# Optimization experiments

Measured on AMD Instinct MI355X. Metric: run time of the kernel, lower is better.

## Reference

```python
import jax, jax.numpy as jnp
import numpy as np
import math

NUM_HEADS = 16
SIZE = 1024
HEAD_SIZE = SIZE // NUM_HEADS
B, S = 2, 2048


def setup_inputs() -> dict:
    key = jax.random.key(0)
    ks = jax.random.split(key, 11)
    sc = 1.0 / math.sqrt(SIZE)
    inp = {
        "q": jax.random.normal(ks[0], (B, S, SIZE), dtype=jnp.float32),
        "k": jax.random.normal(ks[1], (B, S, SIZE), dtype=jnp.float32),
        "v": jax.random.normal(ks[2], (B, S, SIZE), dtype=jnp.float32),
        "Wq": jax.random.normal(ks[3], (SIZE, SIZE), dtype=jnp.float32) * sc,
        "bq": jax.random.normal(ks[4], (SIZE,), dtype=jnp.float32) * sc,
        "Wk": jax.random.normal(ks[5], (SIZE, SIZE), dtype=jnp.float32) * sc,
        "bk": jax.random.normal(ks[6], (SIZE,), dtype=jnp.float32) * sc,
        "Wv": jax.random.normal(ks[7], (SIZE, SIZE), dtype=jnp.float32) * sc,
        "bv": jax.random.normal(ks[8], (SIZE,), dtype=jnp.float32) * sc,
        "Wo": jax.random.normal(ks[9], (SIZE, SIZE), dtype=jnp.float32) * sc,
        "bo": jax.random.normal(ks[10], (SIZE,), dtype=jnp.float32) * sc,
    }
    return inp


def _split_heads(x):
    # [B, S, SIZE] -> [B, H, S, D]
    b, s, _ = x.shape
    return x.reshape(b, s, NUM_HEADS, HEAD_SIZE).transpose(0, 2, 1, 3)


def reference(q, k, v, Wq, bq, Wk, bk, Wv, bv, Wo, bo):
    qh = _split_heads(q @ Wq.T + bq) / math.sqrt(HEAD_SIZE)  # [B,H,S,D]
    kh = _split_heads(k @ Wk.T + bk)
    vh = _split_heads(v @ Wv.T + bv)
    scores = jnp.einsum("bhqd,bhkd->bhqk", qh, kh)  # [B,H,S,S]
    attn = jax.nn.softmax(scores, axis=-1)
    ctx = jnp.einsum("bhqk,bhkd->bhqd", attn, vh)  # [B,H,S,D]
    ctx = ctx.transpose(0, 2, 1, 3).reshape(q.shape[0], -1, SIZE)
    return ctx @ Wo.T + bo
```

## Files before the change

### kernel.cpp

```cpp
#include <hip/hip_runtime.h>
#include <hip/hip_bf16.h>

#define SIZE 1024
#define NH 16
#define HD 64
#define BB 2
#define SS 2048
#define MROWS (BB * SS)
#define QT 128
#define NQT (SS / QT)
#define NKT ((SS / 2) / 64)

using bf16 = __hip_bfloat16;
using frag16 = __attribute__((ext_vector_type(8))) short;
using f32x4 = __attribute__((ext_vector_type(4))) float;
typedef unsigned int u32;

__device__ __forceinline__ void glds16(const bf16* g, bf16* l) {
    __builtin_amdgcn_global_load_lds(
        (const __attribute__((address_space(1))) u32*)g,
        (__attribute__((address_space(3))) u32*)l, 16, 0, 0);
}

__device__ __forceinline__ void cvt_store8(bf16* dst, const float* src) {
    float4 a = *(const float4*)src;
    float4 b = *(const float4*)(src + 4);
    bf16 t[8];
    t[0] = __float2bfloat16(a.x); t[1] = __float2bfloat16(a.y);
    t[2] = __float2bfloat16(a.z); t[3] = __float2bfloat16(a.w);
    t[4] = __float2bfloat16(b.x); t[5] = __float2bfloat16(b.y);
    t[6] = __float2bfloat16(b.z); t[7] = __float2bfloat16(b.w);
    *(uint4*)dst = *(const uint4*)t;
}

__global__ __launch_bounds__(256) void cast_kernel(
    const float* __restrict__ Wq, const float* __restrict__ Wk,
    const float* __restrict__ Wv, const float* __restrict__ Wo,
    const float* __restrict__ q, const float* __restrict__ k,
    const float* __restrict__ v,
    bf16* __restrict__ Wb, bf16* __restrict__ qb,
    bf16* __restrict__ kb, bf16* __restrict__ vb)
{
    const int z = blockIdx.z;
    const float* s; bf16* d; int n;
    switch (z) {
        case 0: s = Wq; d = Wb;                   n = SIZE * SIZE;  break;
        case 1: s = Wk; d = Wb + SIZE * SIZE;     n = SIZE * SIZE;  break;
        case 2: s = Wv; d = Wb + 2 * SIZE * SIZE; n = SIZE * SIZE;  break;
        case 3: s = Wo; d = Wb + 3 * SIZE * SIZE; n = SIZE * SIZE;  break;
        case 4: s = q;  d = qb;                   n = MROWS * SIZE; break;
        case 5: s = k;  d = kb;                   n = MROWS * SIZE; break;
        default: s = v; d = vb;                   n = MROWS * SIZE; break;
    }
    const int i = (blockIdx.x * 256 + threadIdx.x) * 8;
    if (i < n) cvt_store8(d + i, s + i);
}

__device__ __forceinline__ void gemm_body(
    const bf16* __restrict__ X, const bf16* __restrict__ W,
    const float* __restrict__ bias, bf16* __restrict__ Y, float scale, bool vt_mode)
{
    __shared__ __align__(16) bf16 smem[8704];
    bf16* As = smem;
    bf16* Bs = smem + 4096;

    const int tid = threadIdx.x;
    const int wave = tid >> 6;
    const int lane = tid & 63;
    const int lane15 = lane & 15;
    const int quad = lane >> 4;
    const int bm = blockIdx.y * 128;
    const int bn = blockIdx.x * 128;
    const int wm = (wave & 1) * 64;
    const int wn = (wave >> 1) * 64;

    f32x4 acc[4][4];
#pragma unroll
    for (int i = 0; i < 4; i++)
#pragma unroll
        for (int j = 0; j < 4; j++)
            acc[i][j] = (f32x4){0.f, 0.f, 0.f, 0.f};

    const int srow = lane >> 2;
    const int scol = (lane & 3) * 8;

    for (int kt = 0; kt < SIZE / 32; kt++) {
        const int k0 = kt * 32;
        __syncthreads();
#pragma unroll
        for (int n = 0; n < 2; n++) {
            const int c = wave * 2 + n;
            glds16(X + (size_t)(bm + c * 16 + srow) * SIZE + k0 + scol, As + c * 512);
            glds16(W + (size_t)(bn + c * 16 + srow) * SIZE + k0 + scol, Bs + c * 512);
        }
        __syncthreads();

        frag16 a[4], b[4];
#pragma unroll
        for (int mi = 0; mi < 4; mi++)
            a[mi] = *(const frag16*)(As + (wm + mi * 16 + lane15) * 32 + quad * 8);
#pragma unroll
        for (int ni = 0; ni < 4; ni++)
            b[ni] = *(const frag16*)(Bs + (wn + ni * 16 + lane15) * 32 + quad * 8);
#pragma unroll
        for (int mi = 0; mi < 4; mi++)
#pragma unroll
            for (int ni = 0; ni < 4; ni++)
                acc[mi][ni] = __builtin_amdgcn_mfma_f32_16x16x32_bf16(
                    a[mi], b[ni], acc[mi][ni], 0, 0, 0);
    }

    if (!vt_mode) {
#pragma unroll
        for (int ni = 0; ni < 4; ni++) {
            const int col = bn + wn + ni * 16 + lane15;
            const float bv = bias[col];
#pragma unroll
            for (int mi = 0; mi < 4; mi++) {
                const int row = bm + wm + mi * 16 + quad * 4;
#pragma unroll
                for (int r = 0; r < 4; r++)
                    Y[(size_t)(row + r) * SIZE + col] =
                        __float2bfloat16((acc[mi][ni][r] + bv) * scale);
            }
        }
    } else {
        bf16* tr = smem;
        const int bloc = bm >> 11;
        const int s0g = bm & (SS - 1);
#pragma unroll
        for (int p = 0; p < 2; p++) {
            __syncthreads();
            if ((wave >> 1) == p) {
#pragma unroll
                for (int ni = 0; ni < 4; ni++) {
                    const int colp = ni * 16 + lane15;
                    const float bv = bias[bn + p * 64 + colp];
#pragma unroll
                    for (int mi = 0; mi < 4; mi++) {
                        const int row = wm + mi * 16 + quad * 4;
#pragma unroll
                        for (int r = 0; r < 4; r++)
                            tr[colp * 136 + row + r] =
                                __float2bfloat16(acc[mi][ni][r] + bv);
                    }
                }
            }
            __syncthreads();
            const int colp = tid >> 2;
            const int gcol = bn + p * 64 + colp;
            const int hh = gcol >> 6, dd = gcol & (HD - 1);
            bf16* dst = (bf16*)Y + ((size_t)(bloc * NH + hh) * HD + dd) * SS
                        + s0g + (tid & 3) * 32;
            const bf16* src = tr + colp * 136 + (tid & 3) * 32;
#pragma unroll
            for (int j = 0; j < 4; j++)
                *(uint4*)(dst + j * 8) = *(const uint4*)(src + j * 8);
        }
    }
}

__global__ __launch_bounds__(256) void qkv_proj_kernel(
    const bf16* __restrict__ qb, const bf16* __restrict__ kb, const bf16* __restrict__ vb,
    const bf16* __restrict__ Wb,
    const float* __restrict__ bq, const float* __restrict__ bk, const float* __restrict__ bv,
    bf16* __restrict__ qh, bf16* __restrict__ kh, bf16* __restrict__ vt)
{
    const bf16 *X, *W; const float* bi; bf16* Y; float sc; bool vm;
    if (blockIdx.z == 0)      { X = qb; W = Wb;                   bi = bq; Y = qh; sc = 0.125f; vm = false; }
    else if (blockIdx.z == 1) { X = kb; W = Wb + SIZE * SIZE;     bi = bk; Y = kh; sc = 1.0f;   vm = false; }
    else                      { X = vb; W = Wb + 2 * SIZE * SIZE; bi = bv; Y = vt; sc = 1.0f;   vm = true;  }
    gemm_body(X, W, bi, Y, sc, vm);
}

__global__ __launch_bounds__(256) void attn_kernel(
    const bf16* __restrict__ qh, const bf16* __restrict__ kh,
    const bf16* __restrict__ vt, bf16* __restrict__ po, float* __restrict__ pl)
{
    __shared__ __align__(16) bf16 Ks[64][72];
    __shared__ __align__(16) bf16 Vs[64][72];
    __shared__ __align__(16) bf16 Ps[4][32][72];

    const int tid = threadIdx.x;
    const int wave = tid >> 6;
    const int lane = tid & 63;
    const int lane15 = lane & 15;
    const int quad = lane >> 4;

    const int b = blockIdx.z, h = blockIdx.y;
    const int qt = blockIdx.x >> 1;
    const int sh = blockIdx.x & 1;
    const int q0 = qt * QT;

    const size_t baseq = (size_t)b * SS * SIZE + (size_t)h * HD;
    const size_t basev = (size_t)(b * NH + h) * HD * SS;
    const float LOG2E = 1.44269504088896340736f;
    const float OFF = 12.0f * LOG2E;

    frag16 aq[2][2];
#pragma unroll
    for (int m = 0; m < 2; m++) {
        const int qrow = q0 + wave * 32 + m * 16 + lane15;
        const bf16* qp = qh + baseq + (size_t)qrow * SIZE + quad * 8;
        aq[m][0] = *(const frag16*)(qp);
        aq[m][1] = *(const frag16*)(qp + 32);
    }

    frag16 bones;
#pragma unroll
    for (int e = 0; e < 8; e++) bones[e] = (short)0x3F80;

    f32x4 ofrag[2][4], l_frag[2];
#pragma unroll
    for (int m = 0; m < 2; m++) {
        l_frag[m] = (f32x4){0.f, 0.f, 0.f, 0.f};
#pragma unroll
        for (int dt = 0; dt < 4; dt++) ofrag[m][dt] = (f32x4){0.f, 0.f, 0.f, 0.f};
    }

    const int sr = tid >> 3;
    const int sc = (tid & 7) * 8;

    for (int kt = 0; kt < NKT; kt++) {
        const int s0 = sh * (SS / 2) + kt * 64;
        __syncthreads();
        *(uint4*)&Ks[sr][sc]      = *(const uint4*)(kh + baseq + (size_t)(s0 + sr) * SIZE + sc);
        *(uint4*)&Ks[sr + 32][sc] = *(const uint4*)(kh + baseq + (size_t)(s0 + sr + 32) * SIZE + sc);
        *(uint4*)&Vs[sr][sc]      = *(const uint4*)(vt + basev + (size_t)sr * SS + s0 + sc);
        *(uint4*)&Vs[sr + 32][sc] = *(const uint4*)(vt + basev + (size_t)(sr + 32) * SS + s0 + sc);
        __syncthreads();

        frag16 kf[4][2];
#pragma unroll
        for (int nt = 0; nt < 4; nt++) {
            kf[nt][0] = *(const frag16*)&Ks[nt * 16 + lane15][quad * 8];
            kf[nt][1] = *(const frag16*)&Ks[nt * 16 + lane15][32 + quad * 8];
        }
#pragma unroll
        for (int m = 0; m < 2; m++) {
#pragma unroll
            for (int nt = 0; nt < 4; nt++) {
                f32x4 c = (f32x4){0.f, 0.f, 0.f, 0.f};
                c = __builtin_amdgcn_mfma_f32_16x16x32_bf16(kf[nt][0], aq[m][0], c, 0, 0, 0);
                c = __builtin_amdgcn_mfma_f32_16x16x32_bf16(kf[nt][1], aq[m][1], c, 0, 0, 0);
                bf16 p4[4];
#pragma unroll
                for (int r = 0; r < 4; r++)
                    p4[r] = __float2bfloat16(exp2f(fminf(c[r], 30.f) * LOG2E - OFF));
                *(uint2*)&Ps[wave][m * 16 + lane15][nt * 16 + quad * 4] = *(const uint2*)p4;
            }
        }
        __builtin_amdgcn_wave_barrier();

        frag16 ap[2][2];
#pragma unroll
        for (int m = 0; m < 2; m++)
#pragma unroll
            for (int c2 = 0; c2 < 2; c2++)
                ap[m][c2] = *(const frag16*)&Ps[wave][m * 16 + lane15][c2 * 32 + quad * 8];

#pragma unroll
        for (int m = 0; m < 2; m++)
#pragma unroll
            for (int c2 = 0; c2 < 2; c2++)
                l_frag[m] = __builtin_amdgcn_mfma_f32_16x16x32_bf16(
                    ap[m][c2], bones, l_frag[m], 0, 0, 0);

#pragma unroll
        for (int dt = 0; dt < 4; dt++) {
            frag16 bv0 = *(const frag16*)&Vs[dt * 16 + lane15][quad * 8];
            frag16 bv1 = *(const frag16*)&Vs[dt * 16 + lane15][32 + quad * 8];
#pragma unroll
            for (int m = 0; m < 2; m++) {
                ofrag[m][dt] = __builtin_amdgcn_mfma_f32_16x16x32_bf16(ap[m][0], bv0, ofrag[m][dt], 0, 0, 0);
                ofrag[m][dt] = __builtin_amdgcn_mfma_f32_16x16x32_bf16(ap[m][1], bv1, ofrag[m][dt], 0, 0, 0);
            }
        }
    }

    const int pb = ((b * NH + h) * NQT + qt) * 2 + sh;
    if (lane15 == 0) {
        float* plp = pl + (size_t)pb * QT;
#pragma unroll
        for (int m = 0; m < 2; m++)
#pragma unroll
            for (int r = 0; r < 4; r++)
                plp[wave * 32 + m * 16 + quad * 4 + r] = l_frag[m][r];
    }
    bf16* pop = po + (size_t)pb * QT * HD;
#pragma unroll
    for (int m = 0; m < 2; m++)
#pragma unroll
        for (int dt = 0; dt < 4; dt++)
#pragma unroll
            for (int r = 0; r < 4; r++)
                pop[(size_t)(wave * 32 + m * 16 + quad * 4 + r) * HD + dt * 16 + lane15] =
                    __float2bfloat16(ofrag[m][dt][r]);
}

__global__ __launch_bounds__(256) void combine_kernel(
    const bf16* __restrict__ po, const float* __restrict__ pl, bf16* __restrict__ ctx)
{
    const int b = blockIdx.z, h = blockIdx.y, qt = blockIdx.x;
    const int tile = (b * NH + h) * NQT + qt;
    const bf16* p0 = po + (size_t)(tile * 2 + 0) * QT * HD;
    const bf16* p1 = po + (size_t)(tile * 2 + 1) * QT * HD;
    const int qr = threadIdx.x >> 1;
    const int dh = (threadIdx.x & 1) * 32;
    const float l = pl[(size_t)(tile * 2) * QT + qr] + pl[(size_t)(tile * 2 + 1) * QT + qr];
    const float inv = 1.0f / fmaxf(l, 1e-30f);
    bf16* dst = ctx + ((size_t)b * SS + qt * QT + qr) * SIZE + h * HD + dh;
    const bf16* s0p = p0 + qr * HD + dh;
    const bf16* s1p = p1 + qr * HD + dh;
#pragma unroll
    for (int j = 0; j < 32; j += 8) {
        uint4 u0 = *(const uint4*)(s0p + j);
        uint4 u1 = *(const uint4*)(s1p + j);
        const bf16* a = (const bf16*)&u0;
        const bf16* bt = (const bf16*)&u1;
        bf16 o[8];
#pragma unroll
        for (int e = 0; e < 8; e++)
            o[e] = __float2bfloat16((__bfloat162float(a[e]) + __bfloat162float(bt[e])) * inv);
        *(uint4*)(dst + j) = *(const uint4*)o;
    }
}

__global__ __launch_bounds__(256) void out_proj_kernel(
    const bf16* __restrict__ ctx, const bf16* __restrict__ Wob,
    const float* __restrict__ bo, float* __restrict__ out)
{
    __shared__ __align__(16) bf16 As[64 * 32];
    __shared__ __align__(16) bf16 Bs[128 * 32];

    const int tid = threadIdx.x;
    const int wave = tid >> 6;
    const int lane = tid & 63;
    const int lane15 = lane & 15;
    const int quad = lane >> 4;
    const int bm = blockIdx.y * 64;
    const int bn = blockIdx.x * 128;
    const int wn = wave * 32;

    f32x4 acc[4][2];
#pragma unroll
    for (int i = 0; i < 4; i++)
#pragma unroll
        for (int j = 0; j < 2; j++)
            acc[i][j] = (f32x4){0.f, 0.f, 0.f, 0.f};

    const int srow = lane >> 2;
    const int scol = (lane & 3) * 8;

    for (int kt = 0; kt < SIZE / 32; kt++) {
        const int k0 = kt * 32;
        __syncthreads();
        glds16(ctx + (size_t)(bm + wave * 16 + srow) * SIZE + k0 + scol, As + wave * 512);
#pragma unroll
        for (int n = 0; n < 2; n++) {
            const int c = wave * 2 + n;
            glds16(Wob + (size_t)(bn + c * 16 + srow) * SIZE + k0 + scol, Bs + c * 512);
        }
        __syncthreads();

        frag16 a[4], b[2];
#pragma unroll
        for (int mi = 0; mi < 4; mi++)
            a[mi] = *(const frag16*)(As + (mi * 16 + lane15) * 32 + quad * 8);
#pragma unroll
        for (int ni = 0; ni < 2; ni++)
            b[ni] = *(const frag16*)(Bs + (wn + ni * 16 + lane15) * 32 + quad * 8);
#pragma unroll
        for (int mi = 0; mi < 4; mi++)
#pragma unroll
            for (int ni = 0; ni < 2; ni++)
                acc[mi][ni] = __builtin_amdgcn_mfma_f32_16x16x32_bf16(
                    a[mi], b[ni], acc[mi][ni], 0, 0, 0);
    }

#pragma unroll
    for (int ni = 0; ni < 2; ni++) {
        const int col = bn + wn + ni * 16 + lane15;
        const float bv = bo[col];
#pragma unroll
        for (int mi = 0; mi < 4; mi++) {
            const int row = bm + mi * 16 + quad * 4;
#pragma unroll
            for (int r = 0; r < 4; r++)
                out[(size_t)(row + r) * SIZE + col] = acc[mi][ni][r] + bv;
        }
    }
}

extern "C" void kernel_launch(void* const* d_in, const int* in_sizes, int n_in,
                              void* d_out, int out_size, void* d_ws, size_t ws_size,
                              hipStream_t stream) {
    const float* q  = (const float*)d_in[0];
    const float* k  = (const float*)d_in[1];
    const float* v  = (const float*)d_in[2];
    const float* Wq = (const float*)d_in[3];
    const float* bq = (const float*)d_in[4];
    const float* Wk = (const float*)d_in[5];
    const float* bk = (const float*)d_in[6];
    const float* Wv = (const float*)d_in[7];
    const float* bv = (const float*)d_in[8];
    const float* Wo = (const float*)d_in[9];
    const float* bo = (const float*)d_in[10];
    float* out = (float*)d_out;

    bf16* Wb  = (bf16*)d_ws;
    bf16* qb  = Wb + (size_t)4 * SIZE * SIZE;
    bf16* kb  = qb + (size_t)MROWS * SIZE;
    bf16* vb  = kb + (size_t)MROWS * SIZE;
    bf16* qh  = vb + (size_t)MROWS * SIZE;
    bf16* kh  = qh + (size_t)MROWS * SIZE;
    bf16* vt  = kh + (size_t)MROWS * SIZE;
    bf16* po  = qb;
    bf16* ctx = vb;
    float* pl = (float*)Wb;

    cast_kernel<<<dim3(MROWS * SIZE / 2048, 1, 7), 256, 0, stream>>>(
        Wq, Wk, Wv, Wo, q, k, v, Wb, qb, kb, vb);
    qkv_proj_kernel<<<dim3(SIZE / 128, MROWS / 128, 3), 256, 0, stream>>>(
        qb, kb, vb, Wb, bq, bk, bv, qh, kh, vt);
    attn_kernel<<<dim3(NQT * 2, NH, BB), 256, 0, stream>>>(qh, kh, vt, po, pl);
    combine_kernel<<<dim3(NQT, NH, BB), 256, 0, stream>>>(po, pl, ctx);
    out_proj_kernel<<<dim3(SIZE / 128, MROWS / 64, 1), 256, 0, stream>>>(
        ctx, Wb + (size_t)3 * SIZE * SIZE, bo, out);
}
```

Measured before the change: 262.0 us.

## Keep softmax probabilities in registers using 16x16x16 MFMA instead of LDS roundtrip

The exponentiated score tile now goes straight from the QK^T MFMA output layout into the A operand of 16x16x16 bf16 MFMAs for the row-sum and PV products. This drops the per-wave Ps shared buffer, its stores and reloads, and the wave barrier. The cost is twice as many, smaller MFMA instructions (K=16 instead of K=32), which have lower throughput per instruction, plus narrower 8-byte V fragment reads from LDS.

```diff
diff --git a/kernel.cpp b/kernel.cpp
--- a/kernel.cpp
+++ b/kernel.cpp
@@ -13,6 +13,7 @@
 
 using bf16 = __hip_bfloat16;
 using frag16 = __attribute__((ext_vector_type(8))) short;
+using frag4 = __attribute__((ext_vector_type(4))) short;
 using f32x4 = __attribute__((ext_vector_type(4))) float;
 typedef unsigned int u32;
 
@@ -179,7 +180,6 @@
 {
     __shared__ __align__(16) bf16 Ks[64][72];
     __shared__ __align__(16) bf16 Vs[64][72];
-    __shared__ __align__(16) bf16 Ps[4][32][72];
 
     const int tid = threadIdx.x;
     const int wave = tid >> 6;
@@ -206,9 +206,9 @@
         aq[m][1] = *(const frag16*)(qp + 32);
     }
 
-    frag16 bones;
-#pragma unroll
-    for (int e = 0; e < 8; e++) bones[e] = (short)0x3F80;
+    frag4 ones4;
+#pragma unroll
+    for (int e = 0; e < 4; e++) ones4[e] = (short)0x3F80;
 
     f32x4 ofrag[2][4], l_frag[2];
 #pragma unroll
@@ -230,50 +230,35 @@
         *(uint4*)&Vs[sr + 32][sc] = *(const uint4*)(vt + basev + (size_t)(sr + 32) * SS + s0 + sc);
         __syncthreads();
 
-        frag16 kf[4][2];
 #pragma unroll
         for (int nt = 0; nt < 4; nt++) {
-            kf[nt][0] = *(const frag16*)&Ks[nt * 16 + lane15][quad * 8];
-            kf[nt][1] = *(const frag16*)&Ks[nt * 16 + lane15][32 + quad * 8];
-        }
-#pragma unroll
-        for (int m = 0; m < 2; m++) {
-#pragma unroll
-            for (int nt = 0; nt < 4; nt++) {
+            const frag16 kf0 = *(const frag16*)&Ks[nt * 16 + lane15][quad * 8];
+            const frag16 kf1 = *(const frag16*)&Ks[nt * 16 + lane15][32 + quad * 8];
+            frag4 pf[2];
+#pragma unroll
+            for (int m = 0; m < 2; m++) {
                 f32x4 c = (f32x4){0.f, 0.f, 0.f, 0.f};
-                c = __builtin_amdgcn_mfma_f32_16x16x32_bf16(kf[nt][0], aq[m][0], c, 0, 0, 0);
-                c = __builtin_amdgcn_mfma_f32_16x16x32_bf16(kf[nt][1], aq[m][1], c, 0, 0, 0);
+                c = __builtin_amdgcn_mfma_f32_16x16x32_bf16(kf0, aq[m][0], c, 0, 0, 0);
+                c = __builtin_amdgcn_mfma_f32_16x16x32_bf16(kf1, aq[m][1], c, 0, 0, 0);
                 bf16 p4[4];
 #pragma unroll
                 for (int r = 0; r < 4; r++)
                     p4[r] = __float2bfloat16(exp2f(fminf(c[r], 30.f) * LOG2E - OFF));
-                *(uint2*)&Ps[wave][m * 16 + lane15][nt * 16 + quad * 4] = *(const uint2*)p4;
+                pf[m] = *(const frag4*)p4;
             }
-        }
-        __builtin_amdgcn_wave_barrier();
-
-        frag16 ap[2][2];
-#pragma unroll
-        for (int m = 0; m < 2; m++)
-#pragma unroll
-            for (int c2 = 0; c2 < 2; c2++)
-                ap[m][c2] = *(const frag16*)&Ps[wave][m * 16 + lane15][c2 * 32 + quad * 8];
-
-#pragma unroll
-        for (int m = 0; m < 2; m++)
-#pragma unroll
-            for (int c2 = 0; c2 < 2; c2++)
-                l_frag[m] = __builtin_amdgcn_mfma_f32_16x16x32_bf16(
-                    ap[m][c2], bones, l_frag[m], 0, 0, 0);
-
-#pragma unroll
-        for (int dt = 0; dt < 4; dt++) {
-            frag16 bv0 = *(const frag16*)&Vs[dt * 16 + lane15][quad * 8];
-            frag16 bv1 = *(const frag16*)&Vs[dt * 16 + lane15][32 + quad * 8];
-#pragma unroll
-            for (int m = 0; m < 2; m++) {
-                ofrag[m][dt] = __builtin_amdgcn_mfma_f32_16x16x32_bf16(ap[m][0], bv0, ofrag[m][dt], 0, 0, 0);
-                ofrag[m][dt] = __builtin_amdgcn_mfma_f32_16x16x32_bf16(ap[m][1], bv1, ofrag[m][dt], 0, 0, 0);
+
+#pragma unroll
+            for (int m = 0; m < 2; m++)
+                l_frag[m] = __builtin_amdgcn_mfma_f32_16x16x16bf16_1k(
+                    pf[m], ones4, l_frag[m], 0, 0, 0);
+
+#pragma unroll
+            for (int dt = 0; dt < 4; dt++) {
+                const frag4 vf = *(const frag4*)&Vs[dt * 16 + lane15][nt * 16 + quad * 4];
+#pragma unroll
+                for (int m = 0; m < 2; m++)
+                    ofrag[m][dt] = __builtin_amdgcn_mfma_f32_16x16x16bf16_1k(
+                        pf[m], vf, ofrag[m][dt], 0, 0, 0);
             }
         }
     }
```

New measurement: 286.9 us. +9.5%, slower.
